# Kernel tuning notes

Measured on AMD Instinct MI355X. Metric: run time of the kernel, lower is better.

Reference implementation:

```python
import jax, jax.numpy as jnp
import numpy as np

DIM = 1024
HEADS = 16
SCALE = DIM ** (-0.5)  # NOTE: module scales by full dim, not head_dim


def setup_inputs() -> dict:
    key = jax.random.key(0)
    k1, k2, k3, k4 = jax.random.split(key, 4)
    x = jax.random.normal(k1, (4, 2048, DIM), dtype=jnp.float32)
    # torch Linear weights: y = x @ W.T
    w_qkv = jax.random.normal(k2, (3 * DIM, DIM), dtype=jnp.float32) * (DIM ** -0.5)
    w_out = jax.random.normal(k3, (DIM, DIM), dtype=jnp.float32) * (DIM ** -0.5)
    b_out = jax.random.normal(k4, (DIM,), dtype=jnp.float32) * 0.01
    return {"x": x, "w_qkv": w_qkv, "w_out": w_out, "b_out": b_out}


def reference(x, w_qkv, w_out, b_out):
    b, n, _ = x.shape
    h = HEADS
    d = DIM // h
    qkv = x @ w_qkv.T                                   # [b, n, 3*dim]
    qkv = qkv.reshape(b, n, 3, h, d)                    # split (qkv h d)
    qkv = jnp.transpose(qkv, (2, 0, 3, 1, 4))           # [3, b, h, n, d]
    q, k, v = qkv[0], qkv[1], qkv[2]
    dots = jnp.einsum('bhid,bhjd->bhij', q, k) * SCALE  # [b, h, n, n]
    attn = jax.nn.softmax(dots, axis=-1)
    out = jnp.einsum('bhij,bhjd->bhid', attn, v)        # [b, h, n, d]
    out = jnp.transpose(out, (0, 2, 1, 3)).reshape(b, n, h * d)
    return out @ w_out.T + b_out
```

## Files before the change

### kernel.cpp

```cpp
#include <hip/hip_runtime.h>

typedef short bf16x8 __attribute__((ext_vector_type(8)));
typedef _Float16 f16x8 __attribute__((ext_vector_type(8)));
typedef __fp16 fp16x2 __attribute__((ext_vector_type(2)));
typedef float f32x4 __attribute__((ext_vector_type(4)));
typedef float f32x16 __attribute__((ext_vector_type(16)));
typedef unsigned u32x2 __attribute__((ext_vector_type(2)));

static __device__ __forceinline__ unsigned short f2bf(float f) {
  union { float f; unsigned u; } v; v.f = f;
  unsigned r = v.u + 0x7fffu + ((v.u >> 16) & 1u);
  return (unsigned short)(r >> 16);
}

static __device__ __forceinline__ unsigned short f2h(float f) {
  union { _Float16 h; unsigned short u; } c; c.h = (_Float16)f; return c.u;
}

static __device__ __forceinline__ unsigned pkh(float lo, float hi) {
  union { fp16x2 h; unsigned u; } c;
  c.h = __builtin_amdgcn_cvt_pkrtz(lo, hi);
  return c.u;
}

static __device__ __forceinline__ void gll16(const unsigned short* g,
                                             unsigned short* l) {
  __builtin_amdgcn_global_load_lds(
      (const __attribute__((address_space(1))) unsigned int*)g,
      (__attribute__((address_space(3))) unsigned int*)l, 16, 0, 0);
}

__global__ void cvt3_kernel(const float* __restrict__ a,
                            const float* __restrict__ b,
                            const float* __restrict__ c,
                            unsigned short* __restrict__ dst) {
  int i = blockIdx.x * blockDim.x + threadIdx.x;
  const float* src; int off;
  if (i < 2097152) { src = a; off = 0; }
  else if (i < 2883584) { src = b; off = 2097152; }
  else { src = c; off = 2883584; }
  float4 f = ((const float4*)src)[i - off];
  ushort4 o;
  o.x = f2bf(f.x); o.y = f2bf(f.y); o.z = f2bf(f.z); o.w = f2bf(f.w);
  ((ushort4*)dst)[i] = o;
}

#define TM 128
#define TN 128
#define BK 64

template <int EPI>
__global__ __launch_bounds__(256, 2)
void gemm_bt(const unsigned short* __restrict__ X,
             const unsigned short* __restrict__ W,
             unsigned short* __restrict__ QKV, float* __restrict__ OUT,
             const float* __restrict__ bias, int M, int N, int K) {
  __shared__ __align__(16) unsigned short As[TM * BK];
  __shared__ __align__(16) unsigned short Bs[TN * BK];

  const int tid = threadIdx.x;
  const int lane = tid & 63;
  const int wave = tid >> 6;
  const int quad = lane >> 4;
  const int l16 = lane & 15;
  const int wm = wave >> 1, wn = wave & 1;
  const int rc = l16 & 7;

  const int m0 = blockIdx.y * TM;
  const int n0 = blockIdx.x * TN;

  const int sr = lane >> 3;
  const int gsc = ((lane & 7) ^ sr) * 8;

  f32x4 zero = {0.f, 0.f, 0.f, 0.f};
  f32x4 acc[4][4];
#pragma unroll
  for (int i = 0; i < 4; i++)
#pragma unroll
    for (int j = 0; j < 4; j++) acc[i][j] = zero;

  for (int k0 = 0; k0 < K; k0 += BK) {
    __syncthreads();
#pragma unroll
    for (int c = 0; c < 4; c++) {
      int row = wave * 32 + c * 8;
      gll16(&X[(size_t)(m0 + row + sr) * K + k0 + gsc], &As[row * BK]);
      gll16(&W[(size_t)(n0 + row + sr) * K + k0 + gsc], &Bs[row * BK]);
    }
    __syncthreads();
#pragma unroll
    for (int kk = 0; kk < 2; kk++) {
      bf16x8 af[4], bfr[4];
      const int csw = ((kk * 4 + quad) ^ rc) * 8;
#pragma unroll
      for (int t = 0; t < 4; t++) {
        af[t]  = *(const bf16x8*)&As[(wm * 64 + t * 16 + l16) * BK + csw];
        bfr[t] = *(const bf16x8*)&Bs[(wn * 64 + t * 16 + l16) * BK + csw];
      }
#pragma unroll
      for (int mt = 0; mt < 4; mt++)
#pragma unroll
        for (int nt = 0; nt < 4; nt++)
          acc[mt][nt] = __builtin_amdgcn_mfma_f32_16x16x32_bf16(
              af[mt], bfr[nt], acc[mt][nt], 0, 0, 0);
    }
  }

#pragma unroll
  for (int mt = 0; mt < 4; mt++) {
#pragma unroll
    for (int nt = 0; nt < 4; nt++) {
      if (EPI == 0) {
        int nbase = n0 + wn * 64 + nt * 16;
        int which = nbase >> 10;
        if (which == 2) {
          int rem = (nbase + l16) & 1023;
          int h = rem >> 6, dd = rem & 63;
          int growb = m0 + wm * 64 + mt * 16 + quad * 4;
          int b = growb >> 11, nn0 = growb & 2047;
          ushort4 o;
          o.x = f2h(acc[mt][nt][0]);
          o.y = f2h(acc[mt][nt][1]);
          o.z = f2h(acc[mt][nt][2]);
          o.w = f2h(acc[mt][nt][3]);
          *(ushort4*)&QKV[16777216u + (((size_t)(b * 16 + h) * 64 + dd) << 11) + nn0] = o;
        } else {
#pragma unroll
          for (int r = 0; r < 4; r++) {
            int grow = m0 + wm * 64 + mt * 16 + quad * 4 + r;
            int gcol = nbase + l16;
            int rem = gcol & 1023;
            int h = rem >> 6, dd = rem & 63;
            float v = acc[mt][nt][r];
            if (which == 0) v *= 0.04508422f;
            int b = grow >> 11, nn = grow & 2047;
            QKV[(size_t)which * 8388608 +
                ((size_t)(b * 16 + h) * 2048 + nn) * 64 + dd] = f2bf(v);
          }
        }
      } else {
#pragma unroll
        for (int r = 0; r < 4; r++) {
          int grow = m0 + wm * 64 + mt * 16 + quad * 4 + r;
          int gcol = n0 + wn * 64 + nt * 16 + l16;
          OUT[(size_t)grow * N + gcol] = acc[mt][nt][r] + bias[gcol];
        }
      }
    }
  }
}

#define SK 72

__global__ __launch_bounds__(256, 2)
void attn_kernel(const unsigned short* __restrict__ Qg,
                 const unsigned short* __restrict__ Kg,
                 const unsigned short* __restrict__ Vg,
                 unsigned short* __restrict__ AO) {
  __shared__ __align__(16) unsigned short K_s[2][64 * SK];
  __shared__ __align__(16) unsigned short V_s[2][64 * SK];

  const int tid = threadIdx.x;
  const int lane = tid & 63;
  const int wave = tid >> 6;
  const int l31 = lane & 31;
  const int hh = lane >> 5;

  const int qb = blockIdx.x;
  const int bh = blockIdx.y;
  const size_t base = (size_t)bh * 131072;
  const int q0 = qb * 256 + wave * 64;

  bf16x8 bq[2][4];
#pragma unroll
  for (int mt = 0; mt < 2; mt++)
#pragma unroll
    for (int ks = 0; ks < 4; ks++)
      bq[mt][ks] = *(const bf16x8*)&Qg[base + (size_t)(q0 + mt * 32 + l31) * 64 +
                                       ks * 16 + hh * 8];

  f32x16 O[2][2];
#pragma unroll
  for (int mt = 0; mt < 2; mt++)
#pragma unroll
    for (int dt = 0; dt < 2; dt++)
#pragma unroll
      for (int r = 0; r < 16; r++) O[mt][dt][r] = 0.f;
  float lrow[2] = {0.f, 0.f};

  const int sr = lane >> 3, sc = (lane & 7) * 8;
  const unsigned short* Kp = Kg + base + (size_t)(wave * 16 + sr) * 64 + sc;
  const unsigned short* Vp = Vg + base + (size_t)(wave * 16 + sr) * 2048 + sc;
  const int woff = (wave * 16 + sr) * SK + sc;

  uint4 kr0, kr1, vr0, vr1;
  kr0 = *(const uint4*)Kp;           kr1 = *(const uint4*)(Kp + 512);
  vr0 = *(const uint4*)Vp;           vr1 = *(const uint4*)(Vp + 16384);
  *(uint4*)&K_s[0][woff] = kr0;      *(uint4*)&K_s[0][woff + 8 * SK] = kr1;
  *(uint4*)&V_s[0][woff] = vr0;      *(uint4*)&V_s[0][woff + 8 * SK] = vr1;
  __syncthreads();

  for (int t = 0; t < 32; t++) {
    const unsigned short* Kc = K_s[t & 1];
    const unsigned short* Vc = V_s[t & 1];
    if (t < 31) {
      const unsigned short* kp = Kp + (size_t)(t + 1) * 4096;
      const unsigned short* vp = Vp + (size_t)(t + 1) * 64;
      kr0 = *(const uint4*)kp;  kr1 = *(const uint4*)(kp + 512);
      vr0 = *(const uint4*)vp;  vr1 = *(const uint4*)(vp + 16384);
    }

    f32x16 S[2][2];
#pragma unroll
    for (int sub = 0; sub < 2; sub++) {
      f32x16 a0, a1;
#pragma unroll
      for (int r = 0; r < 16; r++) { a0[r] = 0.f; a1[r] = 0.f; }
#pragma unroll
      for (int ks = 0; ks < 4; ks++) {
        bf16x8 kf = *(const bf16x8*)&Kc[(sub * 32 + l31) * SK + ks * 16 + hh * 8];
        a0 = __builtin_amdgcn_mfma_f32_32x32x16_bf16(kf, bq[0][ks], a0, 0, 0, 0);
        a1 = __builtin_amdgcn_mfma_f32_32x32x16_bf16(kf, bq[1][ks], a1, 0, 0, 0);
      }
      S[sub][0] = a0; S[sub][1] = a1;
    }

#pragma unroll
    for (int mt = 0; mt < 2; mt++) {
      float rsum = 0.f;
#pragma unroll
      for (int sub = 0; sub < 2; sub++)
#pragma unroll
        for (int r = 0; r < 16; r++) {
          float p = __builtin_amdgcn_exp2f(S[sub][mt][r]);
          S[sub][mt][r] = p;
          rsum += p;
        }
      lrow[mt] += rsum;
    }

#pragma unroll
    for (int win = 0; win < 4; win++) {
      const int sub = win >> 1, kk = win & 1;
      const int g0 = kk * 2, g1 = kk * 2 + 1;
      f16x8 pf[2];
#pragma unroll
      for (int mt = 0; mt < 2; mt++) {
        unsigned a00 = pkh(S[sub][mt][4 * g0 + 0], S[sub][mt][4 * g0 + 1]);
        unsigned a01 = pkh(S[sub][mt][4 * g0 + 2], S[sub][mt][4 * g0 + 3]);
        unsigned a10 = pkh(S[sub][mt][4 * g1 + 0], S[sub][mt][4 * g1 + 1]);
        unsigned a11 = pkh(S[sub][mt][4 * g1 + 2], S[sub][mt][4 * g1 + 3]);
        union { unsigned u[4]; f16x8 v; } fr;
#if __has_builtin(__builtin_amdgcn_permlane32_swap)
        u32x2 r0 = __builtin_amdgcn_permlane32_swap(a00, a10, false, false);
        u32x2 r1 = __builtin_amdgcn_permlane32_swap(a01, a11, false, false);
        fr.u[0] = r0.x; fr.u[1] = r1.x; fr.u[2] = r0.y; fr.u[3] = r1.y;
#else
        unsigned b00 = __shfl_xor((int)a00, 32);
        unsigned b01 = __shfl_xor((int)a01, 32);
        unsigned b10 = __shfl_xor((int)a10, 32);
        unsigned b11 = __shfl_xor((int)a11, 32);
        fr.u[0] = hh ? b10 : a00;
        fr.u[1] = hh ? b11 : a01;
        fr.u[2] = hh ? a10 : b00;
        fr.u[3] = hh ? a11 : b01;
#endif
        pf[mt] = fr.v;
      }
#pragma unroll
      for (int dt = 0; dt < 2; dt++) {
        f16x8 vf = *(const f16x8*)&Vc[(dt * 32 + l31) * SK + win * 16 + hh * 8];
#pragma unroll
        for (int mt = 0; mt < 2; mt++)
          O[mt][dt] = __builtin_amdgcn_mfma_f32_32x32x16_f16(vf, pf[mt], O[mt][dt], 0, 0, 0);
      }
    }

    if (t < 31) {
      const int nb = (t + 1) & 1;
      *(uint4*)&K_s[nb][woff] = kr0;  *(uint4*)&K_s[nb][woff + 8 * SK] = kr1;
      *(uint4*)&V_s[nb][woff] = vr0;  *(uint4*)&V_s[nb][woff + 8 * SK] = vr1;
    }
    __syncthreads();
  }

  const int b4 = bh >> 4, head = bh & 15;
#pragma unroll
  for (int mt = 0; mt < 2; mt++) {
    lrow[mt] += __shfl_xor(lrow[mt], 32);
    float inv = 1.0f / lrow[mt];
    int row = b4 * 2048 + q0 + mt * 32 + l31;
#pragma unroll
    for (int dt = 0; dt < 2; dt++)
#pragma unroll
      for (int g = 0; g < 4; g++) {
        ushort4 o;
        o.x = f2bf(O[mt][dt][4 * g + 0] * inv);
        o.y = f2bf(O[mt][dt][4 * g + 1] * inv);
        o.z = f2bf(O[mt][dt][4 * g + 2] * inv);
        o.w = f2bf(O[mt][dt][4 * g + 3] * inv);
        *(ushort4*)&AO[(size_t)row * 1024 + head * 64 + dt * 32 + 8 * g + 4 * hh] = o;
      }
  }
}

extern "C" void kernel_launch(void* const* d_in, const int* in_sizes, int n_in,
                              void* d_out, int out_size, void* d_ws,
                              size_t ws_size, hipStream_t stream) {
  const float* x     = (const float*)d_in[0];
  const float* w_qkv = (const float*)d_in[1];
  const float* w_out = (const float*)d_in[2];
  const float* b_out = (const float*)d_in[3];
  float* out = (float*)d_out;

  unsigned short* ws = (unsigned short*)d_ws;
  unsigned short* Xbf  = ws;
  unsigned short* Wqkv = ws + 8388608;
  unsigned short* Wout = ws + 11534336;
  unsigned short* QKV  = ws + 12582912;
  unsigned short* AO   = ws;

  cvt3_kernel<<<12288, 256, 0, stream>>>(x, w_qkv, w_out, Xbf);

  gemm_bt<0><<<dim3(3072 / TN, 8192 / TM), 256, 0, stream>>>(
      Xbf, Wqkv, QKV, nullptr, nullptr, 8192, 3072, 1024);

  attn_kernel<<<dim3(8, 64), 256, 0, stream>>>(
      QKV, QKV + 8388608, QKV + 16777216, AO);

  gemm_bt<1><<<dim3(1024 / TN, 8192 / TM), 256, 0, stream>>>(
      AO, Wout, nullptr, out, b_out, 8192, 1024, 1024);
}
```

Before: 250.9 us.

## Use 8 waves of 32 query rows per attention block with XCD-aware block mapping

New measurement: 251.2 us. Within noise of the previous version (+0.1%).

```diff
diff --git a/kernel.cpp b/kernel.cpp
--- a/kernel.cpp
+++ b/kernel.cpp
@@ -152,7 +152,7 @@
 
 #define SK 72
 
-__global__ __launch_bounds__(256, 2)
+__global__ __launch_bounds__(512, 4)
 void attn_kernel(const unsigned short* __restrict__ Qg,
                  const unsigned short* __restrict__ Kg,
                  const unsigned short* __restrict__ Vg,
@@ -166,142 +166,126 @@
   const int l31 = lane & 31;
   const int hh = lane >> 5;
 
-  const int qb = blockIdx.x;
-  const int bh = blockIdx.y;
+  const int id = blockIdx.x + 8 * blockIdx.y;
+  const int xcd = id & 7;
+  const int slot = id >> 3;
+  const int bh = xcd * 8 + (slot & 7);
+  const int qb = slot >> 3;
+
   const size_t base = (size_t)bh * 131072;
-  const int q0 = qb * 256 + wave * 64;
-
-  bf16x8 bq[2][4];
-#pragma unroll
-  for (int mt = 0; mt < 2; mt++)
-#pragma unroll
-    for (int ks = 0; ks < 4; ks++)
-      bq[mt][ks] = *(const bf16x8*)&Qg[base + (size_t)(q0 + mt * 32 + l31) * 64 +
-                                       ks * 16 + hh * 8];
-
-  f32x16 O[2][2];
-#pragma unroll
-  for (int mt = 0; mt < 2; mt++)
-#pragma unroll
-    for (int dt = 0; dt < 2; dt++)
-#pragma unroll
-      for (int r = 0; r < 16; r++) O[mt][dt][r] = 0.f;
-  float lrow[2] = {0.f, 0.f};
+  const int q0 = qb * 256 + wave * 32;
+
+  bf16x8 bq[4];
+#pragma unroll
+  for (int ks = 0; ks < 4; ks++)
+    bq[ks] = *(const bf16x8*)&Qg[base + (size_t)(q0 + l31) * 64 + ks * 16 + hh * 8];
+
+  f32x16 O[2];
+#pragma unroll
+  for (int dt = 0; dt < 2; dt++)
+#pragma unroll
+    for (int r = 0; r < 16; r++) O[dt][r] = 0.f;
+  float lrow = 0.f;
 
   const int sr = lane >> 3, sc = (lane & 7) * 8;
-  const unsigned short* Kp = Kg + base + (size_t)(wave * 16 + sr) * 64 + sc;
-  const unsigned short* Vp = Vg + base + (size_t)(wave * 16 + sr) * 2048 + sc;
-  const int woff = (wave * 16 + sr) * SK + sc;
-
-  uint4 kr0, kr1, vr0, vr1;
-  kr0 = *(const uint4*)Kp;           kr1 = *(const uint4*)(Kp + 512);
-  vr0 = *(const uint4*)Vp;           vr1 = *(const uint4*)(Vp + 16384);
-  *(uint4*)&K_s[0][woff] = kr0;      *(uint4*)&K_s[0][woff + 8 * SK] = kr1;
-  *(uint4*)&V_s[0][woff] = vr0;      *(uint4*)&V_s[0][woff + 8 * SK] = vr1;
+  const unsigned short* Kp = Kg + base + (size_t)(wave * 8 + sr) * 64 + sc;
+  const unsigned short* Vp = Vg + base + (size_t)(wave * 8 + sr) * 2048 + sc;
+  const int woff = (wave * 8 + sr) * SK + sc;
+
+  uint4 kr, vr;
+  kr = *(const uint4*)Kp;
+  vr = *(const uint4*)Vp;
+  *(uint4*)&K_s[0][woff] = kr;
+  *(uint4*)&V_s[0][woff] = vr;
   __syncthreads();
 
   for (int t = 0; t < 32; t++) {
     const unsigned short* Kc = K_s[t & 1];
     const unsigned short* Vc = V_s[t & 1];
     if (t < 31) {
-      const unsigned short* kp = Kp + (size_t)(t + 1) * 4096;
-      const unsigned short* vp = Vp + (size_t)(t + 1) * 64;
-      kr0 = *(const uint4*)kp;  kr1 = *(const uint4*)(kp + 512);
-      vr0 = *(const uint4*)vp;  vr1 = *(const uint4*)(vp + 16384);
-    }
-
-    f32x16 S[2][2];
+      kr = *(const uint4*)(Kp + (size_t)(t + 1) * 4096);
+      vr = *(const uint4*)(Vp + (size_t)(t + 1) * 64);
+    }
+
+    f32x16 S[2];
 #pragma unroll
     for (int sub = 0; sub < 2; sub++) {
-      f32x16 a0, a1;
-#pragma unroll
-      for (int r = 0; r < 16; r++) { a0[r] = 0.f; a1[r] = 0.f; }
+      f32x16 a;
+#pragma unroll
+      for (int r = 0; r < 16; r++) a[r] = 0.f;
 #pragma unroll
       for (int ks = 0; ks < 4; ks++) {
         bf16x8 kf = *(const bf16x8*)&Kc[(sub * 32 + l31) * SK + ks * 16 + hh * 8];
-        a0 = __builtin_amdgcn_mfma_f32_32x32x16_bf16(kf, bq[0][ks], a0, 0, 0, 0);
-        a1 = __builtin_amdgcn_mfma_f32_32x32x16_bf16(kf, bq[1][ks], a1, 0, 0, 0);
-      }
-      S[sub][0] = a0; S[sub][1] = a1;
-    }
-
-#pragma unroll
-    for (int mt = 0; mt < 2; mt++) {
-      float rsum = 0.f;
-#pragma unroll
-      for (int sub = 0; sub < 2; sub++)
-#pragma unroll
-        for (int r = 0; r < 16; r++) {
-          float p = __builtin_amdgcn_exp2f(S[sub][mt][r]);
-          S[sub][mt][r] = p;
-          rsum += p;
-        }
-      lrow[mt] += rsum;
-    }
+        a = __builtin_amdgcn_mfma_f32_32x32x16_bf16(kf, bq[ks], a, 0, 0, 0);
+      }
+      S[sub] = a;
+    }
+
+    float rsum = 0.f;
+#pragma unroll
+    for (int sub = 0; sub < 2; sub++)
+#pragma unroll
+      for (int r = 0; r < 16; r++) {
+        float p = __builtin_amdgcn_exp2f(S[sub][r]);
+        S[sub][r] = p;
+        rsum += p;
+      }
+    lrow += rsum;
 
 #pragma unroll
     for (int win = 0; win < 4; win++) {
       const int sub = win >> 1, kk = win & 1;
       const int g0 = kk * 2, g1 = kk * 2 + 1;
-      f16x8 pf[2];
-#pragma unroll
-      for (int mt = 0; mt < 2; mt++) {
-        unsigned a00 = pkh(S[sub][mt][4 * g0 + 0], S[sub][mt][4 * g0 + 1]);
-        unsigned a01 = pkh(S[sub][mt][4 * g0 + 2], S[sub][mt][4 * g0 + 3]);
-        unsigned a10 = pkh(S[sub][mt][4 * g1 + 0], S[sub][mt][4 * g1 + 1]);
-        unsigned a11 = pkh(S[sub][mt][4 * g1 + 2], S[sub][mt][4 * g1 + 3]);
-        union { unsigned u[4]; f16x8 v; } fr;
+      unsigned a00 = pkh(S[sub][4 * g0 + 0], S[sub][4 * g0 + 1]);
+      unsigned a01 = pkh(S[sub][4 * g0 + 2], S[sub][4 * g0 + 3]);
+      unsigned a10 = pkh(S[sub][4 * g1 + 0], S[sub][4 * g1 + 1]);
+      unsigned a11 = pkh(S[sub][4 * g1 + 2], S[sub][4 * g1 + 3]);
+      union { unsigned u[4]; f16x8 v; } fr;
 #if __has_builtin(__builtin_amdgcn_permlane32_swap)
-        u32x2 r0 = __builtin_amdgcn_permlane32_swap(a00, a10, false, false);
-        u32x2 r1 = __builtin_amdgcn_permlane32_swap(a01, a11, false, false);
-        fr.u[0] = r0.x; fr.u[1] = r1.x; fr.u[2] = r0.y; fr.u[3] = r1.y;
+      u32x2 r0 = __builtin_amdgcn_permlane32_swap(a00, a10, false, false);
+      u32x2 r1 = __builtin_amdgcn_permlane32_swap(a01, a11, false, false);
+      fr.u[0] = r0.x; fr.u[1] = r1.x; fr.u[2] = r0.y; fr.u[3] = r1.y;
 #else
-        unsigned b00 = __shfl_xor((int)a00, 32);
-        unsigned b01 = __shfl_xor((int)a01, 32);
-        unsigned b10 = __shfl_xor((int)a10, 32);
-        unsigned b11 = __shfl_xor((int)a11, 32);
-        fr.u[0] = hh ? b10 : a00;
-        fr.u[1] = hh ? b11 : a01;
-        fr.u[2] = hh ? a10 : b00;
-        fr.u[3] = hh ? a11 : b01;
+      unsigned b00 = __shfl_xor((int)a00, 32);
+      unsigned b01 = __shfl_xor((int)a01, 32);
+      unsigned b10 = __shfl_xor((int)a10, 32);
+      unsigned b11 = __shfl_xor((int)a11, 32);
+      fr.u[0] = hh ? b10 : a00;
+      fr.u[1] = hh ? b11 : a01;
+      fr.u[2] = hh ? a10 : b00;
+      fr.u[3] = hh ? a11 : b01;
 #endif
-        pf[mt] = fr.v;
-      }
+      f16x8 pf = fr.v;
 #pragma unroll
       for (int dt = 0; dt < 2; dt++) {
         f16x8 vf = *(const f16x8*)&Vc[(dt * 32 + l31) * SK + win * 16 + hh * 8];
-#pragma unroll
-        for (int mt = 0; mt < 2; mt++)
-          O[mt][dt] = __builtin_amdgcn_mfma_f32_32x32x16_f16(vf, pf[mt], O[mt][dt], 0, 0, 0);
+        O[dt] = __builtin_amdgcn_mfma_f32_32x32x16_f16(vf, pf, O[dt], 0, 0, 0);
       }
     }
 
     if (t < 31) {
       const int nb = (t + 1) & 1;
-      *(uint4*)&K_s[nb][woff] = kr0;  *(uint4*)&K_s[nb][woff + 8 * SK] = kr1;
-      *(uint4*)&V_s[nb][woff] = vr0;  *(uint4*)&V_s[nb][woff + 8 * SK] = vr1;
+      *(uint4*)&K_s[nb][woff] = kr;
+      *(uint4*)&V_s[nb][woff] = vr;
     }
     __syncthreads();
   }
 
   const int b4 = bh >> 4, head = bh & 15;
-#pragma unroll
-  for (int mt = 0; mt < 2; mt++) {
-    lrow[mt] += __shfl_xor(lrow[mt], 32);
-    float inv = 1.0f / lrow[mt];
-    int row = b4 * 2048 + q0 + mt * 32 + l31;
-#pragma unroll
-    for (int dt = 0; dt < 2; dt++)
-#pragma unroll
-      for (int g = 0; g < 4; g++) {
-        ushort4 o;
-        o.x = f2bf(O[mt][dt][4 * g + 0] * inv);
-        o.y = f2bf(O[mt][dt][4 * g + 1] * inv);
-        o.z = f2bf(O[mt][dt][4 * g + 2] * inv);
-        o.w = f2bf(O[mt][dt][4 * g + 3] * inv);
-        *(ushort4*)&AO[(size_t)row * 1024 + head * 64 + dt * 32 + 8 * g + 4 * hh] = o;
-      }
-  }
+  lrow += __shfl_xor(lrow, 32);
+  float inv = 1.0f / lrow;
+  int row = b4 * 2048 + q0 + l31;
+#pragma unroll
+  for (int dt = 0; dt < 2; dt++)
+#pragma unroll
+    for (int g = 0; g < 4; g++) {
+      ushort4 o;
+      o.x = f2bf(O[dt][4 * g + 0] * inv);
+      o.y = f2bf(O[dt][4 * g + 1] * inv);
+      o.z = f2bf(O[dt][4 * g + 2] * inv);
+      o.w = f2bf(O[dt][4 * g + 3] * inv);
+      *(ushort4*)&AO[(size_t)row * 1024 + head * 64 + dt * 32 + 8 * g + 4 * hh] = o;
+    }
 }
 
 extern "C" void kernel_launch(void* const* d_in, const int* in_sizes, int n_in,
@@ -325,7 +309,7 @@
   gemm_bt<0><<<dim3(3072 / TN, 8192 / TM), 256, 0, stream>>>(
       Xbf, Wqkv, QKV, nullptr, nullptr, 8192, 3072, 1024);
 
-  attn_kernel<<<dim3(8, 64), 256, 0, stream>>>(
+  attn_kernel<<<dim3(8, 64), 512, 0, stream>>>(
       QKV, QKV + 8388608, QKV + 16777216, AO);
 
   gemm_bt<1><<<dim3(1024 / TN, 8192 / TM), 256, 0, stream>>>(
```
